# Kernel tuning notes

Hardware: AMD Instinct MI355X
Metric: run time of the kernel (lower is better)

The kernel has to match this reference:

```python
import jax, jax.numpy as jnp
import numpy as np

GROUPS = 8
EPS = 1e-5


def group_norm(x, gamma, beta):
    # x: [B,H,W,C]; normalize per group over (H, W, C/g)
    B, H, W, C = x.shape
    g = GROUPS
    xg = x.reshape(B, H, W, g, C // g)
    mean = jnp.mean(xg, axis=(1, 2, 4), keepdims=True)
    var = jnp.var(xg, axis=(1, 2, 4), keepdims=True)
    xg = (xg - mean) / jnp.sqrt(var + EPS)
    return gamma * xg.reshape(B, H, W, C) + beta


def setup_inputs() -> dict:
    key = jax.random.key(0)
    ks = jax.random.split(key, 6)
    B, H, W, C = 8, 64, 64, 128
    s = 1.0 / np.sqrt(C)
    return {
        "x": jax.random.normal(ks[0], (B, H, W, C), jnp.float32),
        "gamma": jnp.ones((C,), jnp.float32),
        "beta": jnp.zeros((C,), jnp.float32),
        "wq": jax.random.normal(ks[1], (C, C), jnp.float32) * s,
        "bq": jnp.zeros((C,), jnp.float32),
        "wk": jax.random.normal(ks[2], (C, C), jnp.float32) * s,
        "bk": jnp.zeros((C,), jnp.float32),
        "wv": jax.random.normal(ks[3], (C, C), jnp.float32) * s,
        "bv": jnp.zeros((C,), jnp.float32),
        "wp": jax.random.normal(ks[4], (C, C), jnp.float32) * s,
        "bp": jnp.zeros((C,), jnp.float32),
    }


def reference(x, gamma, beta, wq, bq, wk, bk, wv, bv, wp, bp):
    B, H, W, C = x.shape
    scale = jnp.asarray(C, jnp.float32) ** -0.5
    xn = group_norm(x, gamma, beta)  # note: residual uses normalized input (as in source)
    N = H * W
    xf = xn.reshape(B, N, C)
    q = xf @ wq + bq
    k = xf @ wk + bk
    v = xf @ wv + bv
    attn = jnp.einsum('bnc,bmc->bnm', q, k) * scale  # [B, N, N]
    attn = jax.nn.softmax(attn, axis=-1)
    out = jnp.einsum('bnm,bmc->bnc', attn, v)
    out = out @ wp + bp
    return (xf + out).reshape(B, H, W, C)
```

## Files before the change

### kernel.cpp

```cpp
#include <hip/hip_runtime.h>
#include <hip/hip_bf16.h>

#define B_ 8
#define N_ 4096
#define C_ 128
#define EPSV 1e-5f
#define SPLIT 2
#define KVB 64

using bf8   = __attribute__((ext_vector_type(8))) short;
using u16x8 = __attribute__((ext_vector_type(8))) ushort;
using f32x4 = __attribute__((ext_vector_type(4))) float;

__device__ __forceinline__ ushort f2b(float f) {
  __hip_bfloat16 h = __float2bfloat16(f);
  return *reinterpret_cast<ushort*>(&h);
}
__device__ __forceinline__ float b2f(ushort u) {
  union { float f; unsigned x; } t; t.x = ((unsigned)u) << 16; return t.f;
}

__device__ __forceinline__ void gll16(const void* g, void* l) {
  __builtin_amdgcn_global_load_lds((const __attribute__((address_space(1))) void*)g,
                                   (__attribute__((address_space(3))) void*)l,
                                   16, 0, 0);
}

__global__ __launch_bounds__(256) void gnw(const float* __restrict__ x,
                                           const float* __restrict__ wq,
                                           const float* __restrict__ wk,
                                           const float* __restrict__ wv,
                                           const float* __restrict__ wp,
                                           float2* __restrict__ part,
                                           ushort* __restrict__ wt) {
  if (blockIdx.y >= 64) {
    const int widx = blockIdx.y - 64;
    const float* w = (widx == 0) ? wq : (widx == 1) ? wk : (widx == 2) ? wv : wp;
    ushort* o = wt + widx * 16384;
    const int r  = blockIdx.x * 16 + (threadIdx.x >> 4);
    const int c0 = (threadIdx.x & 15) << 3;
    const float4 v0 = *reinterpret_cast<const float4*>(w + (size_t)r * C_ + c0);
    const float4 v1 = *reinterpret_cast<const float4*>(w + (size_t)r * C_ + c0 + 4);
    const float vv[8] = {v0.x, v0.y, v0.z, v0.w, v1.x, v1.y, v1.z, v1.w};
    #pragma unroll
    for (int j = 0; j < 8; ++j) {
      const int n = c0 + j;
      const int el = (r & 7) | ((((r >> 3)) ^ (n & 7)) << 3);
      o[(size_t)n * C_ + el] = f2b(vv[j]);
    }
    return;
  }
  const int bg = blockIdx.y;
  const int b = bg >> 3, g = bg & 7;
  const int chunk = blockIdx.x;
  const float* xp = x + (size_t)b * N_ * C_ + g * 16;
  float s = 0.f, s2 = 0.f;
  const int base4 = chunk * 2048;
  for (int i = threadIdx.x; i < 2048; i += 256) {
    const int idx = base4 + i;
    const int n = idx >> 2, c4 = (idx & 3) << 2;
    const float4 v = *reinterpret_cast<const float4*>(xp + (size_t)n * C_ + c4);
    s  += v.x + v.y + v.z + v.w;
    s2 += v.x*v.x + v.y*v.y + v.z*v.z + v.w*v.w;
  }
  #pragma unroll
  for (int off = 32; off; off >>= 1) { s += __shfl_down(s, off); s2 += __shfl_down(s2, off); }
  __shared__ float red[8];
  const int wid = threadIdx.x >> 6;
  if ((threadIdx.x & 63) == 0) { red[wid] = s; red[4 + wid] = s2; }
  __syncthreads();
  if (threadIdx.x == 0)
    part[bg * 8 + chunk] = make_float2(red[0]+red[1]+red[2]+red[3],
                                       red[4]+red[5]+red[6]+red[7]);
}

__device__ __forceinline__ void block_mrs(const float2* part, int b, int tid,
                                          float2* sp, float* mrs) {
  if (tid < 64) sp[tid] = part[b * 64 + tid];
  __syncthreads();
  if (tid < 8) {
    float s = 0.f, s2 = 0.f;
    #pragma unroll
    for (int c = 0; c < 8; ++c) { s += sp[tid*8+c].x; s2 += sp[tid*8+c].y; }
    const float inv = 1.f / 65536.f;
    const float m = s * inv;
    const float var = s2 * inv - m * m;
    mrs[tid*2]   = m;
    mrs[tid*2+1] = rsqrtf(var + EPSV);
  }
  __syncthreads();
}

__global__ __launch_bounds__(256) void qkv_fused(const float* __restrict__ x,
                                                 const float2* __restrict__ part,
                                                 const float* __restrict__ gamma,
                                                 const float* __restrict__ beta,
                                                 const ushort* __restrict__ wt,
                                                 const float* __restrict__ bq,
                                                 const float* __restrict__ bk,
                                                 const float* __restrict__ bv,
                                                 ushort* __restrict__ qb, ushort* __restrict__ kb,
                                                 ushort* __restrict__ vtb) {
  __shared__ ushort A[64][128];
  __shared__ ushort Bt[128][128];
  __shared__ float2 sp[64];
  __shared__ float mrs[16];
  const int m0 = blockIdx.x * 64;
  const int tid = threadIdx.x;
  const int wid = tid >> 6, lane = tid & 63;
  block_mrs(part, m0 >> 12, tid, sp, mrs);
  for (int i = tid; i < 1024; i += 256) {
    const int row = i >> 4, c = (i & 15) << 3;
    const int grow = m0 + row;
    const float mm = mrs[(c >> 4) * 2], rr = mrs[(c >> 4) * 2 + 1];
    const float4 v0 = *reinterpret_cast<const float4*>(&x[(size_t)grow * C_ + c]);
    const float4 v1 = *reinterpret_cast<const float4*>(&x[(size_t)grow * C_ + c + 4]);
    const float vv[8] = {v0.x, v0.y, v0.z, v0.w, v1.x, v1.y, v1.z, v1.w};
    u16x8 u;
    #pragma unroll
    for (int j = 0; j < 8; ++j)
      u[j] = f2b((vv[j] - mm) * rr * gamma[c+j] + beta[c+j]);
    const int el = ((c >> 3) ^ (row & 7)) << 3;
    *reinterpret_cast<u16x8*>(&A[row][el]) = u;
  }
  const int wm = wid >> 1, wn = wid & 1;
  const int lr = lane & 15, lk = lane >> 4;
  const float qscale = 0.12751749f;

  #pragma unroll 1
  for (int j = 0; j < 3; ++j) {
    const ushort* wtj = wt + j * 16384;
    const float* bias = (j == 0) ? bq : (j == 1) ? bk : bv;
    __syncthreads();
    {
      ushort* bt0 = &Bt[0][0];
      #pragma unroll
      for (int c8 = 0; c8 < 8; ++c8) {
        const int ch = wid * 8 + c8;
        gll16(wtj + ch * 512 + lane * 8, bt0 + ch * 512);
      }
    }
    __syncthreads();
    f32x4 acc[2][4] = {};
    #pragma unroll
    for (int ks = 0; ks < 4; ++ks) {
      const int g0 = ks * 4 + lk;
      bf8 af[2], bfv[4];
      #pragma unroll
      for (int mi = 0; mi < 2; ++mi) {
        const int row = wm * 32 + mi * 16 + lr;
        af[mi] = *reinterpret_cast<const bf8*>(&A[row][(g0 ^ (row & 7)) << 3]);
      }
      #pragma unroll
      for (int ni = 0; ni < 4; ++ni) {
        const int n = wn * 64 + ni * 16 + lr;
        bfv[ni] = *reinterpret_cast<const bf8*>(&Bt[n][(g0 ^ (n & 7)) << 3]);
      }
      #pragma unroll
      for (int mi = 0; mi < 2; ++mi)
        #pragma unroll
        for (int ni = 0; ni < 4; ++ni)
          acc[mi][ni] = __builtin_amdgcn_mfma_f32_16x16x32_bf16(af[mi], bfv[ni], acc[mi][ni], 0, 0, 0);
    }
    if (j < 2) {
      ushort* out = (j == 0) ? qb : kb;
      const float sc = (j == 0) ? qscale : 1.0f;
      #pragma unroll
      for (int mi = 0; mi < 2; ++mi)
        #pragma unroll
        for (int ni = 0; ni < 4; ++ni)
          #pragma unroll
          for (int r = 0; r < 4; ++r) {
            const int row = m0 + wm * 32 + mi * 16 + lk * 4 + r;
            const int col = wn * 64 + ni * 16 + lr;
            out[(size_t)row * C_ + col] = f2b((acc[mi][ni][r] + bias[col]) * sc);
          }
    } else {
      #pragma unroll
      for (int mi = 0; mi < 2; ++mi)
        #pragma unroll
        for (int ni = 0; ni < 4; ++ni) {
          const int rowb = m0 + wm * 32 + mi * 16 + lk * 4;
          const int col  = wn * 64 + ni * 16 + lr;
          const int bb = rowb >> 12, nn = rowb & 4095;
          const float bv2 = bias[col];
          ushort4 u;
          u.x = f2b(acc[mi][ni][0] + bv2);
          u.y = f2b(acc[mi][ni][1] + bv2);
          u.z = f2b(acc[mi][ni][2] + bv2);
          u.w = f2b(acc[mi][ni][3] + bv2);
          *reinterpret_cast<ushort4*>(&vtb[((size_t)bb * C_ + col) * N_ + nn]) = u;
        }
    }
  }
}

__global__ __launch_bounds__(256, 2) void attn_fwd(const ushort* __restrict__ q,
                                                   const ushort* __restrict__ k,
                                                   const ushort* __restrict__ vt,
                                                   ushort* __restrict__ Op,
                                                   float* __restrict__ lsum) {
  extern __shared__ ushort smem[];
  const int bid = blockIdx.x;
  const int b   = bid & 7;
  const int qi  = (bid >> 3) & 31;
  const int z   = bid >> 8;
  const int q0  = qi * 128;
  const int tid = threadIdx.x;
  const int w = tid >> 6, lane = tid & 63;
  const int lr = lane & 15, lk = lane >> 4;
  const ushort* qb = q  + (size_t)b * N_ * C_;
  const ushort* kb = k  + (size_t)b * N_ * C_;
  const ushort* vb = vt + (size_t)b * C_ * N_;

  bf8 qf[2][4];
  #pragma unroll
  for (int h = 0; h < 2; ++h) {
    const int qrow = q0 + w * 32 + h * 16 + lr;
    #pragma unroll
    for (int ks = 0; ks < 4; ++ks)
      qf[h][ks] = *reinterpret_cast<const bf8*>(&qb[(size_t)qrow * C_ + ks * 32 + lk * 8]);
  }

  bf8 onesf;
  #pragma unroll
  for (int j = 0; j < 8; ++j) onesf[j] = (short)0x3F80;

  f32x4 oacc[2][8] = {};
  f32x4 accl[2] = {};

  const int krow_in = lane >> 4;
  const int kslot   = lane & 15;
  const int vrow_in = lane >> 3;
  const int vslot   = lane & 7;

  const int t0 = z * (64 / SPLIT);
  const int t1 = (z + 1) * (64 / SPLIT);

  auto STAGE = [&](int sel, int kt) {
    const int kv0 = kt * KVB;
    ushort* Kd = smem + sel * 8192;
    ushort* Vd = smem + 16384 + sel * 8192;
    #pragma unroll
    for (int j = 0; j < 4; ++j) {
      const int m = w * 4 + j;
      const int krow = m * 4 + krow_in;
      gll16(kb + (size_t)(kv0 + krow) * C_ + ((kslot ^ (krow & 7)) << 3),
            Kd + m * 512);
      const int vrow = m * 8 + vrow_in;
      gll16(vb + (size_t)vrow * N_ + kv0 + ((vslot ^ (vrow & 7)) << 3),
            Vd + m * 512);
    }
  };

  STAGE(0, t0);
  for (int kt = t0; kt < t1; ++kt) {
    const int cur = (kt - t0) & 1;
    __syncthreads();
    if (kt + 1 < t1) STAGE(cur ^ 1, kt + 1);

    const ushort* Kc = smem + cur * 8192;
    const ushort* Vc = smem + 16384 + cur * 8192;
    ushort* Pw = smem + 32768 + w * 2048;

    f32x4 s[2][4] = {};
    __builtin_amdgcn_s_setprio(1);
    #pragma unroll
    for (int ks = 0; ks < 4; ++ks) {
      const int g0 = ks * 4 + lk;
      bf8 kf[4];
      #pragma unroll
      for (int ni = 0; ni < 4; ++ni) {
        const int n = ni * 16 + lr;
        kf[ni] = *reinterpret_cast<const bf8*>(&Kc[n * 128 + ((g0 ^ (n & 7)) << 3)]);
      }
      #pragma unroll
      for (int h = 0; h < 2; ++h)
        #pragma unroll
        for (int ni = 0; ni < 4; ++ni)
          s[h][ni] = __builtin_amdgcn_mfma_f32_16x16x32_bf16(kf[ni], qf[h][ks], s[h][ni], 0, 0, 0);
    }
    __builtin_amdgcn_s_setprio(0);

    #pragma unroll
    for (int h = 0; h < 2; ++h) {
      const int prow = h * 16 + lr;
      ushort* pw = Pw + prow * 64;
      #pragma unroll
      for (int ni = 0; ni < 4; ++ni) {
        const float p0 = __builtin_amdgcn_exp2f(s[h][ni][0]);
        const float p1 = __builtin_amdgcn_exp2f(s[h][ni][1]);
        const float p2 = __builtin_amdgcn_exp2f(s[h][ni][2]);
        const float p3 = __builtin_amdgcn_exp2f(s[h][ni][3]);
        ushort4 u; u.x = f2b(p0); u.y = f2b(p1); u.z = f2b(p2); u.w = f2b(p3);
        const int qd = (ni * 4 + lk) ^ ((lr & 7) << 1);
        *reinterpret_cast<ushort4*>(pw + qd * 4) = u;
      }
    }

    __builtin_amdgcn_s_setprio(1);
    #pragma unroll
    for (int kss = 0; kss < 2; ++kss) {
      bf8 pa[2];
      #pragma unroll
      for (int h = 0; h < 2; ++h) {
        const int g = (kss * 4 + lk) ^ (lr & 7);
        pa[h] = *reinterpret_cast<const bf8*>(&Pw[(h * 16 + lr) * 64 + (g << 3)]);
      }
      #pragma unroll
      for (int h = 0; h < 2; ++h)
        accl[h] = __builtin_amdgcn_mfma_f32_16x16x32_bf16(pa[h], onesf, accl[h], 0, 0, 0);
      #pragma unroll
      for (int ni = 0; ni < 8; ++ni) {
        const int d = ni * 16 + lr;
        const bf8 vf = *reinterpret_cast<const bf8*>(&Vc[d * 64 + (((kss * 4 + lk) ^ (d & 7)) << 3)]);
        #pragma unroll
        for (int h = 0; h < 2; ++h)
          oacc[h][ni] = __builtin_amdgcn_mfma_f32_16x16x32_bf16(pa[h], vf, oacc[h][ni], 0, 0, 0);
      }
    }
    __builtin_amdgcn_s_setprio(0);
  }

  const size_t zb = (size_t)(z * B_ + b);
  if (lr == 0) {
    #pragma unroll
    for (int h = 0; h < 2; ++h)
      #pragma unroll
      for (int r = 0; r < 4; ++r)
        lsum[zb * N_ + q0 + w * 32 + h * 16 + lk * 4 + r] = accl[h][r];
  }
  ushort* ob = Op + zb * N_ * C_;
  #pragma unroll
  for (int h = 0; h < 2; ++h)
    #pragma unroll
    for (int ni = 0; ni < 8; ++ni)
      #pragma unroll
      for (int r = 0; r < 4; ++r) {
        const int row = q0 + w * 32 + h * 16 + lk * 4 + r;
        ob[(size_t)row * C_ + ni * 16 + lr] = f2b(oacc[h][ni][r]);
      }
}

__global__ __launch_bounds__(256) void proj_res(const ushort* __restrict__ Op,
                                                const float* __restrict__ lsum,
                                                const ushort* __restrict__ wtp,
                                                const float* __restrict__ bias,
                                                const float* __restrict__ x,
                                                const float2* __restrict__ part,
                                                const float* __restrict__ gamma,
                                                const float* __restrict__ beta,
                                                float* __restrict__ outp) {
  __shared__ ushort A[64][128];
  __shared__ ushort Bt[128][128];
  __shared__ float2 sp[64];
  __shared__ float mrs[16];
  const int m0 = blockIdx.x * 64;
  const int tid = threadIdx.x;
  const int wid = tid >> 6, lane = tid & 63;
  const size_t BN = (size_t)B_ * N_;
  block_mrs(part, m0 >> 12, tid, sp, mrs);
  {
    ushort* bt0 = &Bt[0][0];
    #pragma unroll
    for (int c8 = 0; c8 < 8; ++c8) {
      const int ch = wid * 8 + c8;
      gll16(wtp + ch * 512 + lane * 8, bt0 + ch * 512);
    }
  }
  for (int i = tid; i < 1024; i += 256) {
    const int row = i >> 4, c = (i & 15) << 3;
    const size_t grow = m0 + row;
    float l = 0.f;
    #pragma unroll
    for (int zz = 0; zz < SPLIT; ++zz) l += lsum[zz * BN + grow];
    const float inv = 1.f / l;
    float acc8[8] = {};
    #pragma unroll
    for (int zz = 0; zz < SPLIT; ++zz) {
      const u16x8 a = *reinterpret_cast<const u16x8*>(&Op[(zz * BN + grow) * C_ + c]);
      #pragma unroll
      for (int j = 0; j < 8; ++j) acc8[j] += b2f(a[j]);
    }
    u16x8 u;
    #pragma unroll
    for (int j = 0; j < 8; ++j) u[j] = f2b(acc8[j] * inv);
    const int el = ((c >> 3) ^ (row & 7)) << 3;
    *reinterpret_cast<u16x8*>(&A[row][el]) = u;
  }
  __syncthreads();
  const int wm = wid >> 1, wn = wid & 1;
  const int lr = lane & 15, lk = lane >> 4;
  f32x4 acc[2][4] = {};
  #pragma unroll
  for (int ks = 0; ks < 4; ++ks) {
    const int g0 = ks * 4 + lk;
    bf8 af[2], bfv[4];
    #pragma unroll
    for (int mi = 0; mi < 2; ++mi) {
      const int row = wm * 32 + mi * 16 + lr;
      af[mi] = *reinterpret_cast<const bf8*>(&A[row][(g0 ^ (row & 7)) << 3]);
    }
    #pragma unroll
    for (int ni = 0; ni < 4; ++ni) {
      const int n = wn * 64 + ni * 16 + lr;
      bfv[ni] = *reinterpret_cast<const bf8*>(&Bt[n][(g0 ^ (n & 7)) << 3]);
    }
    #pragma unroll
    for (int mi = 0; mi < 2; ++mi)
      #pragma unroll
      for (int ni = 0; ni < 4; ++ni)
        acc[mi][ni] = __builtin_amdgcn_mfma_f32_16x16x32_bf16(af[mi], bfv[ni], acc[mi][ni], 0, 0, 0);
  }
  #pragma unroll
  for (int mi = 0; mi < 2; ++mi)
    #pragma unroll
    for (int ni = 0; ni < 4; ++ni) {
      const int col = wn * 64 + ni * 16 + lr;
      const float gmm = gamma[col], bta = beta[col], bia = bias[col];
      const float mm = mrs[(col >> 4) * 2], rr = mrs[(col >> 4) * 2 + 1];
      #pragma unroll
      for (int r = 0; r < 4; ++r) {
        const int row = m0 + wm * 32 + mi * 16 + lk * 4 + r;
        const float xn = (x[(size_t)row * C_ + col] - mm) * rr * gmm + bta;
        outp[(size_t)row * C_ + col] = xn + acc[mi][ni][r] + bia;
      }
    }
}

extern "C" void kernel_launch(void* const* d_in, const int* in_sizes, int n_in,
                              void* d_out, int out_size, void* d_ws, size_t ws_size,
                              hipStream_t stream) {
  const float* x     = (const float*)d_in[0];
  const float* gamma = (const float*)d_in[1];
  const float* beta  = (const float*)d_in[2];
  const float* wq    = (const float*)d_in[3];
  const float* bq    = (const float*)d_in[4];
  const float* wk    = (const float*)d_in[5];
  const float* bk    = (const float*)d_in[6];
  const float* wv    = (const float*)d_in[7];
  const float* bv    = (const float*)d_in[8];
  const float* wp    = (const float*)d_in[9];
  const float* bp    = (const float*)d_in[10];
  float* outp = (float*)d_out;

  char* ws = (char*)d_ws;
  const size_t MB8 = (size_t)B_ * N_ * C_ * 2;
  float2* part = (float2*)(ws + 512);
  ushort* qb   = (ushort*)(ws + 8192);
  ushort* kb   = (ushort*)(ws + 8192 + MB8);
  ushort* vtb  = (ushort*)(ws + 8192 + 2*MB8);
  ushort* Op   = (ushort*)(ws + 8192 + 3*MB8);
  float*  lsum = (float*)(ws + 8192 + (3 + SPLIT)*MB8);
  ushort* wt   = (ushort*)(ws + 8192 + (3 + SPLIT)*MB8 + (size_t)SPLIT*B_*N_*4);

  gnw<<<dim3(8, 68), 256, 0, stream>>>(x, wq, wk, wv, wp, part, wt);
  qkv_fused<<<512, 256, 0, stream>>>(x, part, gamma, beta, wt,
                                     bq, bk, bv, qb, kb, vtb);
  (void)hipFuncSetAttribute((const void*)attn_fwd,
                            hipFuncAttributeMaxDynamicSharedMemorySize, 81920);
  attn_fwd<<<dim3(32 * B_ * SPLIT), 256, 81920, stream>>>(qb, kb, vtb, Op, lsum);
  proj_res<<<512, 256, 0, stream>>>(Op, lsum, wt + 3 * 16384, bp, x, part, gamma, beta, outp);
}
```

Baseline: 101.5 us.

## Keep softmax probabilities in registers and permute V reads to match MFMA layout

```diff
diff --git a/kernel.cpp b/kernel.cpp
--- a/kernel.cpp
+++ b/kernel.cpp
@@ -9,6 +9,7 @@
 #define KVB 64
 
 using bf8   = __attribute__((ext_vector_type(8))) short;
+using bf4   = __attribute__((ext_vector_type(4))) short;
 using u16x8 = __attribute__((ext_vector_type(8))) ushort;
 using f32x4 = __attribute__((ext_vector_type(4))) float;
 
@@ -261,7 +262,6 @@
 
     const ushort* Kc = smem + cur * 8192;
     const ushort* Vc = smem + 16384 + cur * 8192;
-    ushort* Pw = smem + 32768 + w * 2048;
 
     f32x4 s[2][4] = {};
     __builtin_amdgcn_s_setprio(1);
@@ -282,41 +282,40 @@
     }
     __builtin_amdgcn_s_setprio(0);
 
-    #pragma unroll
-    for (int h = 0; h < 2; ++h) {
-      const int prow = h * 16 + lr;
-      ushort* pw = Pw + prow * 64;
-      #pragma unroll
-      for (int ni = 0; ni < 4; ++ni) {
-        const float p0 = __builtin_amdgcn_exp2f(s[h][ni][0]);
-        const float p1 = __builtin_amdgcn_exp2f(s[h][ni][1]);
-        const float p2 = __builtin_amdgcn_exp2f(s[h][ni][2]);
-        const float p3 = __builtin_amdgcn_exp2f(s[h][ni][3]);
-        ushort4 u; u.x = f2b(p0); u.y = f2b(p1); u.z = f2b(p2); u.w = f2b(p3);
-        const int qd = (ni * 4 + lk) ^ ((lr & 7) << 1);
-        *reinterpret_cast<ushort4*>(pw + qd * 4) = u;
-      }
-    }
+    bf8 pa[2][2];
+    #pragma unroll
+    for (int kss = 0; kss < 2; ++kss)
+      #pragma unroll
+      for (int h = 0; h < 2; ++h) {
+        bf8 t;
+        #pragma unroll
+        for (int half = 0; half < 2; ++half) {
+          const f32x4 sv = s[h][kss * 2 + half];
+          #pragma unroll
+          for (int r = 0; r < 4; ++r)
+            t[half * 4 + r] = (short)f2b(__builtin_amdgcn_exp2f(sv[r]));
+        }
+        pa[kss][h] = t;
+      }
 
     __builtin_amdgcn_s_setprio(1);
     #pragma unroll
     for (int kss = 0; kss < 2; ++kss) {
-      bf8 pa[2];
-      #pragma unroll
-      for (int h = 0; h < 2; ++h) {
-        const int g = (kss * 4 + lk) ^ (lr & 7);
-        pa[h] = *reinterpret_cast<const bf8*>(&Pw[(h * 16 + lr) * 64 + (g << 3)]);
-      }
       #pragma unroll
       for (int h = 0; h < 2; ++h)
-        accl[h] = __builtin_amdgcn_mfma_f32_16x16x32_bf16(pa[h], onesf, accl[h], 0, 0, 0);
+        accl[h] = __builtin_amdgcn_mfma_f32_16x16x32_bf16(pa[kss][h], onesf, accl[h], 0, 0, 0);
+      const int gl = kss * 4 + (lk >> 1);
+      const int hf = (lk & 1) << 2;
       #pragma unroll
       for (int ni = 0; ni < 8; ++ni) {
         const int d = ni * 16 + lr;
-        const bf8 vf = *reinterpret_cast<const bf8*>(&Vc[d * 64 + (((kss * 4 + lk) ^ (d & 7)) << 3)]);
+        const int sw = d & 7;
+        const bf4 lo = *reinterpret_cast<const bf4*>(&Vc[d * 64 + ((gl ^ sw) << 3) + hf]);
+        const bf4 hi = *reinterpret_cast<const bf4*>(&Vc[d * 64 + (((gl + 2) ^ sw) << 3) + hf]);
+        const bf8 vf = __builtin_shufflevector(lo, hi, 0, 1, 2, 3, 4, 5, 6, 7);
         #pragma unroll
         for (int h = 0; h < 2; ++h)
-          oacc[h][ni] = __builtin_amdgcn_mfma_f32_16x16x32_bf16(pa[h], vf, oacc[h][ni], 0, 0, 0);
+          oacc[h][ni] = __builtin_amdgcn_mfma_f32_16x16x32_bf16(pa[kss][h], vf, oacc[h][ni], 0, 0, 0);
       }
     }
     __builtin_amdgcn_s_setprio(0);
@@ -458,7 +457,7 @@
   qkv_fused<<<512, 256, 0, stream>>>(x, part, gamma, beta, wt,
                                      bq, bk, bv, qb, kb, vtb);
   (void)hipFuncSetAttribute((const void*)attn_fwd,
-                            hipFuncAttributeMaxDynamicSharedMemorySize, 81920);
-  attn_fwd<<<dim3(32 * B_ * SPLIT), 256, 81920, stream>>>(qb, kb, vtb, Op, lsum);
+                            hipFuncAttributeMaxDynamicSharedMemorySize, 65536);
+  attn_fwd<<<dim3(32 * B_ * SPLIT), 256, 65536, stream>>>(qb, kb, vtb, Op, lsum);
   proj_res<<<512, 256, 0, stream>>>(Op, lsum, wt + 3 * 16384, bp, x, part, gamma, beta, outp);
 }
```

New measurement: 99.77 us. No clear change (-1.7%).
